# Performance work log

Measured on AMD Instinct MI355X. Metric: run time of the kernel, lower is better.

Reference implementation:

```python
import jax, jax.numpy as jnp
import numpy as np

N = 4096; E = 65536; IN = 512; H = 256; QD = 256; NH = 8; HD = QD // NH
OUT = 10; L = 2; CT = 50


def _ln(x, g, b, eps=1e-5):
    mu = x.mean(-1, keepdims=True)
    var = ((x - mu) ** 2).mean(-1, keepdims=True)
    return (x - mu) * jax.lax.rsqrt(var + eps) * g + b


def _forward(x, edge_index, cell_types, Wi, bi, Wq, bq, Wk, bk, Wv, bv, Bc, cemb,
             Win, bin_p, Wo, bo, Wm1, bm1, Wm2, bm2, Wm3, bm3, ln_g, ln_b,
             Wc1, bc1, Wc2, bc2):
    src, tgt = edge_index[0], edge_index[1]
    h = jax.nn.relu(x @ Wi + bi)                      # [N, H] input projection
    # graph connectivity scattered into a dense mask (as in _create_attention_mask)
    mask = jnp.zeros((N, N), jnp.float32).at[src, tgt].set(1.0)
    for l in range(L):
        res = h
        Q = h @ Wq[l] + bq[l]                         # [N, QD]
        K = h @ Wk[l] + bk[l]
        V = h @ Wv[l] + bv[l]
        Q = Q @ Bc[l]                                 # biological constraint
        K = K @ Bc[l].T
        ce = cemb[l][cell_types]                      # [N, QD] cell-type embedding
        Q = Q + 0.1 * ce
        K = K + 0.1 * ce
        # dense graph-masked attention (entanglement matrix), applied to V
        scores = (Q @ K.T) / float(np.sqrt(QD))      # [N, N]
        scores = jnp.where(mask == 0.0, -1e9, scores)
        attn = jax.nn.softmax(scores, axis=-1)
        graph_att = attn @ V                          # [N, QD]
        # nn.MultiheadAttention(Q, K, V) entanglement layer (eval mode)
        q = (Q @ Win[l, :, :QD] + bin_p[l, :QD]).reshape(N, NH, HD)
        k = (K @ Win[l, :, QD:2 * QD] + bin_p[l, QD:2 * QD]).reshape(N, NH, HD)
        v = (V @ Win[l, :, 2 * QD:] + bin_p[l, 2 * QD:]).reshape(N, NH, HD)
        w = jax.nn.softmax(jnp.einsum('nhd,mhd->hnm', q, k) / float(np.sqrt(HD)), axis=-1)
        mha = jnp.einsum('hnm,mhd->nhd', w, v).reshape(N, QD) @ Wo[l] + bo[l]
        # edge gather -> message MLP -> scatter-add (PyG aggr='add', x_i=target, x_j=source)
        # quantum slot of the concat is zeros, so only the first 2H rows of Wm1 contribute
        m = jnp.concatenate([h[tgt], h[src]], axis=-1) @ Wm1[l, :2 * H] + bm1[l]
        m = jax.nn.relu(m)
        m = jax.nn.relu(m @ Wm2[l] + bm2[l])
        m = m @ Wm3[l] + bm3[l]                       # [E, H]
        agg = jax.ops.segment_sum(m, tgt, num_segments=N)
        h = _ln(res + agg + mha + graph_att, ln_g[l], ln_b[l])
    # graph-level readout: mean || max pooling -> classifier (hidden*2 -> hidden -> out)
    pooled = jnp.concatenate([h.mean(0), h.max(0)], axis=-1)   # [2H]
    z = jax.nn.relu(pooled @ Wc1 + bc1)
    return z @ Wc2 + bc2                              # [OUT]


def setup_inputs():
    ks = jax.random.split(jax.random.key(0), 40)
    s = 0.05
    p = lambda i, shape: jax.random.normal(ks[i], shape, jnp.float32) * s
    z = lambda shape: jnp.zeros(shape, jnp.float32)
    return {
        'x': jax.random.normal(ks[0], (N, IN), jnp.float32),
        'edge_index': jax.random.randint(ks[1], (2, E), 0, N),
        'cell_types': jax.random.randint(ks[2], (N,), 0, CT),
        'Wi': p(3, (IN, H)), 'bi': z((H,)),
        'Wq': p(4, (L, H, QD)), 'bq': z((L, QD)),
        'Wk': p(5, (L, H, QD)), 'bk': z((L, QD)),
        'Wv': p(6, (L, H, QD)), 'bv': z((L, QD)),
        'Bc': p(7, (L, QD, QD)),
        'cemb': p(8, (L, CT, QD)),
        'Win': p(9, (L, QD, 3 * QD)), 'bin_p': z((L, 3 * QD)),
        'Wo': p(10, (L, QD, QD)), 'bo': z((L, QD)),
        'Wm1': p(11, (L, 2 * H + QD, QD)), 'bm1': z((L, QD)),
        'Wm2': p(12, (L, QD, QD)), 'bm2': z((L, QD)),
        'Wm3': p(13, (L, QD, H)), 'bm3': z((L, H)),
        'ln_g': jnp.ones((L, H), jnp.float32), 'ln_b': z((L, H)),
        'Wc1': p(14, (2 * H, H)), 'bc1': z((H,)),
        'Wc2': p(15, (H, OUT)), 'bc2': z((OUT,)),
    }


def reference(x, edge_index, cell_types, Wi, bi, Wq, bq, Wk, bk, Wv, bv, Bc, cemb,
              Win, bin_p, Wo, bo, Wm1, bm1, Wm2, bm2, Wm3, bm3, ln_g, ln_b,
              Wc1, bc1, Wc2, bc2):
    return _forward(x, edge_index, cell_types, Wi, bi, Wq, bq, Wk, bk, Wv, bv, Bc, cemb,
                    Win, bin_p, Wo, bo, Wm1, bm1, Wm2, bm2, Wm3, bm3, ln_g, ln_b,
                    Wc1, bc1, Wc2, bc2)
```

## Files before the change

kernel.cpp:

```cpp
#include <hip/hip_runtime.h>
#include <hip/hip_bf16.h>

#define N_NODES 4096
#define E_EDGES 65536
#define IN_F    512
#define H_F     256
#define QD      256
#define NHEAD   8
#define HD      32
#define OUT_F   10
#define L_LAYERS 2
#define CT_N    50

enum { FLAG_RELU = 1, FLAG_ACCUM = 2, FLAG_WF32 = 4, FLAG_WB16 = 8 };

typedef __attribute__((ext_vector_type(8))) __bf16 bf16x8;
typedef __attribute__((ext_vector_type(4))) float f32x4;

union PU { bf16x8 v; __hip_bfloat16 h[8]; __hip_bfloat162 b2[4]; };

template<int BM, int BN, bool EDGE>
__global__ __launch_bounds__(256) void gemm_mfma(
    const __hip_bfloat16* __restrict__ A, int lda,
    const __hip_bfloat16* __restrict__ B, int ldb,
    float* __restrict__ Cf, __hip_bfloat16* __restrict__ Cb, int ldc,
    int K,
    const float* __restrict__ bias, const float* __restrict__ rowscale,
    const int* __restrict__ tgtp, const int* __restrict__ srcp,
    const float* __restrict__ kbias,
    int flags)
{
    constexpr int WM = BM / 2, WN = BN / 2, MT = WM / 16, NT = WN / 16;
    constexpr int LDT = 40;
    __shared__ alignas(16) __hip_bfloat16 As[BM * LDT];
    __shared__ alignas(16) __hip_bfloat16 Bs[BN * LDT];

    const int tid = threadIdx.x;
    const int w = tid >> 6, lane = tid & 63, l16 = lane & 15, quad = lane >> 4;
    const int wm = w >> 1, wn = w & 1;
    const int bm = blockIdx.y * BM, bn = blockIdx.x * BN;

    f32x4 acc[MT][NT];
    #pragma unroll
    for (int i = 0; i < MT; ++i)
        #pragma unroll
        for (int j = 0; j < NT; ++j)
            #pragma unroll
            for (int r = 0; r < 4; ++r) acc[i][j][r] = 0.f;

    for (int k0 = 0; k0 < K; k0 += 32) {
        #pragma unroll
        for (int f = tid; f < BM * 4; f += 256) {
            int r = f >> 2, sg = f & 3;
            if (EDGE) {
                int i = bm + r;
                int tg = tgtp[i], sr = srcp[i];
                PU z1, z2, o;
                z1.v = *reinterpret_cast<const bf16x8*>(A + (size_t)tg * 512 + k0 + sg * 8);
                z2.v = *reinterpret_cast<const bf16x8*>(A + (size_t)sr * 512 + 256 + k0 + sg * 8);
                float4 b0 = *reinterpret_cast<const float4*>(kbias + k0 + sg * 8);
                float4 b1 = *reinterpret_cast<const float4*>(kbias + k0 + sg * 8 + 4);
                float bb[8] = {b0.x, b0.y, b0.z, b0.w, b1.x, b1.y, b1.z, b1.w};
                #pragma unroll
                for (int j = 0; j < 8; ++j) {
                    float v = __bfloat162float(z1.h[j]) + __bfloat162float(z2.h[j]) + bb[j];
                    o.h[j] = __float2bfloat16(fmaxf(v, 0.f));
                }
                *reinterpret_cast<bf16x8*>(&As[r * LDT + sg * 8]) = o.v;
            } else {
                *reinterpret_cast<uint4*>(&As[r * LDT + sg * 8]) =
                    *reinterpret_cast<const uint4*>(A + (size_t)(bm + r) * lda + k0 + sg * 8);
            }
        }
        #pragma unroll
        for (int f = tid; f < BN * 4; f += 256) {
            int r = f >> 2, sg = f & 3;
            *reinterpret_cast<uint4*>(&Bs[r * LDT + sg * 8]) =
                *reinterpret_cast<const uint4*>(B + (size_t)(bn + r) * ldb + k0 + sg * 8);
        }
        __syncthreads();
        bf16x8 af[MT], bfr[NT];
        #pragma unroll
        for (int mt = 0; mt < MT; ++mt)
            af[mt] = *reinterpret_cast<const bf16x8*>(&As[(wm * WM + mt * 16 + l16) * LDT + quad * 8]);
        #pragma unroll
        for (int nt = 0; nt < NT; ++nt)
            bfr[nt] = *reinterpret_cast<const bf16x8*>(&Bs[(wn * WN + nt * 16 + l16) * LDT + quad * 8]);
        #pragma unroll
        for (int mt = 0; mt < MT; ++mt)
            #pragma unroll
            for (int nt = 0; nt < NT; ++nt)
                acc[mt][nt] = __builtin_amdgcn_mfma_f32_16x16x32_bf16(af[mt], bfr[nt], acc[mt][nt], 0, 0, 0);
        __syncthreads();
    }

    #pragma unroll
    for (int mt = 0; mt < MT; ++mt) {
        #pragma unroll
        for (int nt = 0; nt < NT; ++nt) {
            int col = bn + wn * WN + nt * 16 + l16;
            #pragma unroll
            for (int r = 0; r < 4; ++r) {
                int row = bm + wm * WM + mt * 16 + quad * 4 + r;
                float v = acc[mt][nt][r];
                if (bias) {
                    float bv = bias[col];
                    if (rowscale) bv *= rowscale[row];
                    v += bv;
                }
                if (flags & FLAG_RELU) v = fmaxf(v, 0.f);
                size_t off = (size_t)row * ldc + col;
                if (flags & FLAG_ACCUM)     Cf[off] += v;
                else if (flags & FLAG_WF32) Cf[off] = v;
                if (flags & FLAG_WB16)      Cb[off] = __float2bfloat16(v);
            }
        }
    }
}

__global__ __launch_bounds__(512) void edge_gemm(
    const __hip_bfloat16* __restrict__ Z,
    const __hip_bfloat16* __restrict__ B,
    __hip_bfloat16* __restrict__ C,
    const int* __restrict__ tgtp, const int* __restrict__ srcp,
    const float* __restrict__ kbias,
    const float* __restrict__ bias)
{
    constexpr int LDA = 264;
    constexpr int LDB = 40;
    __shared__ alignas(16) __hip_bfloat16 As[64 * LDA];
    __shared__ alignas(16) __hip_bfloat16 Bs[256 * LDB];

    const int tid = threadIdx.x;
    const int w = tid >> 6, lane = tid & 63, l16 = lane & 15, quad = lane >> 4;
    const int bid = blockIdx.x;
    const int bm = ((bid & 7) * 128 + (bid >> 3)) * 64;

    bf16x8 zt[4], zs[4];
    #pragma unroll
    for (int u = 0; u < 4; ++u) {
        int g = u * 512 + tid;
        int r = g >> 5, c = g & 31;
        int i = bm + r;
        int tg = tgtp[i], sr = srcp[i];
        zt[u] = *reinterpret_cast<const bf16x8*>(Z + (size_t)tg * 512 + c * 8);
        zs[u] = *reinterpret_cast<const bf16x8*>(Z + (size_t)sr * 512 + 256 + c * 8);
    }
    #pragma unroll
    for (int u = 0; u < 4; ++u) {
        int g = u * 512 + tid;
        int r = g >> 5, c = g & 31;
        PU a, b, o;
        a.v = zt[u]; b.v = zs[u];
        float4 k0v = *reinterpret_cast<const float4*>(kbias + c * 8);
        float4 k1v = *reinterpret_cast<const float4*>(kbias + c * 8 + 4);
        float bb[8] = {k0v.x, k0v.y, k0v.z, k0v.w, k1v.x, k1v.y, k1v.z, k1v.w};
        #pragma unroll
        for (int j = 0; j < 8; ++j) {
            float v = __bfloat162float(a.h[j]) + __bfloat162float(b.h[j]) + bb[j];
            o.h[j] = __float2bfloat16(fmaxf(v, 0.f));
        }
        *reinterpret_cast<bf16x8*>(&As[r * LDA + c * 8]) = o.v;
    }

    const int wn = w;
    f32x4 acc[4][2];
    #pragma unroll
    for (int mt = 0; mt < 4; ++mt)
        #pragma unroll
        for (int nt = 0; nt < 2; ++nt)
            #pragma unroll
            for (int r = 0; r < 4; ++r) acc[mt][nt][r] = 0.f;

    for (int k0 = 0; k0 < 256; k0 += 32) {
        #pragma unroll
        for (int u = 0; u < 2; ++u) {
            int f = u * 512 + tid;
            int r = f >> 2, sg = f & 3;
            *reinterpret_cast<uint4*>(&Bs[r * LDB + sg * 8]) =
                *reinterpret_cast<const uint4*>(B + (size_t)r * 256 + k0 + sg * 8);
        }
        __syncthreads();
        bf16x8 af[4], bfr[2];
        #pragma unroll
        for (int mt = 0; mt < 4; ++mt)
            af[mt] = *reinterpret_cast<const bf16x8*>(&As[(mt * 16 + l16) * LDA + k0 + quad * 8]);
        #pragma unroll
        for (int nt = 0; nt < 2; ++nt)
            bfr[nt] = *reinterpret_cast<const bf16x8*>(&Bs[(wn * 32 + nt * 16 + l16) * LDB + quad * 8]);
        #pragma unroll
        for (int mt = 0; mt < 4; ++mt)
            #pragma unroll
            for (int nt = 0; nt < 2; ++nt)
                acc[mt][nt] = __builtin_amdgcn_mfma_f32_16x16x32_bf16(af[mt], bfr[nt], acc[mt][nt], 0, 0, 0);
        __syncthreads();
    }

    #pragma unroll
    for (int mt = 0; mt < 4; ++mt) {
        #pragma unroll
        for (int nt = 0; nt < 2; ++nt) {
            int col = wn * 32 + nt * 16 + l16;
            float bv = bias[col];
            #pragma unroll
            for (int r = 0; r < 4; ++r) {
                int row = bm + mt * 16 + quad * 4 + r;
                float v = fmaxf(acc[mt][nt][r] + bv, 0.f);
                C[(size_t)row * 256 + col] = __float2bfloat16(v);
            }
        }
    }
}

struct GSet { const __hip_bfloat16* A; int lda; const __hip_bfloat16* B;
              const float* bias; const float* rowscale;
              const float* extra; float esc; float cscale;
              __hip_bfloat16* C; float* Cf; int vtout; int ldc; int coloff; };
struct GPack { GSet s[8]; };

__global__ __launch_bounds__(256) void gemm_bz(GPack p, const int* __restrict__ eidx)
{
    GSet g = p.s[blockIdx.z];
    constexpr int LDT = 40;
    __shared__ alignas(16) __hip_bfloat16 As[64 * LDT];
    __shared__ alignas(16) __hip_bfloat16 Bs[64 * LDT];

    const int tid = threadIdx.x;
    const int w = tid >> 6, lane = tid & 63, l16 = lane & 15, quad = lane >> 4;
    const int wm = w >> 1, wn = w & 1;
    const int bm = blockIdx.y * 64, bn = blockIdx.x * 64;

    f32x4 acc[2][2];
    #pragma unroll
    for (int i = 0; i < 2; ++i)
        #pragma unroll
        for (int j = 0; j < 2; ++j)
            #pragma unroll
            for (int r = 0; r < 4; ++r) acc[i][j][r] = 0.f;

    for (int k0 = 0; k0 < 256; k0 += 32) {
        #pragma unroll
        for (int f = tid; f < 256; f += 256) {
            int r = f >> 2, sg = f & 3;
            *reinterpret_cast<uint4*>(&As[r * LDT + sg * 8]) =
                *reinterpret_cast<const uint4*>(g.A + (size_t)(bm + r) * g.lda + k0 + sg * 8);
            *reinterpret_cast<uint4*>(&Bs[r * LDT + sg * 8]) =
                *reinterpret_cast<const uint4*>(g.B + (size_t)(bn + r) * 256 + k0 + sg * 8);
        }
        __syncthreads();
        bf16x8 af[2], bfr[2];
        #pragma unroll
        for (int mt = 0; mt < 2; ++mt)
            af[mt] = *reinterpret_cast<const bf16x8*>(&As[(wm * 32 + mt * 16 + l16) * LDT + quad * 8]);
        #pragma unroll
        for (int nt = 0; nt < 2; ++nt)
            bfr[nt] = *reinterpret_cast<const bf16x8*>(&Bs[(wn * 32 + nt * 16 + l16) * LDT + quad * 8]);
        #pragma unroll
        for (int mt = 0; mt < 2; ++mt)
            #pragma unroll
            for (int nt = 0; nt < 2; ++nt)
                acc[mt][nt] = __builtin_amdgcn_mfma_f32_16x16x32_bf16(af[mt], bfr[nt], acc[mt][nt], 0, 0, 0);
        __syncthreads();
    }

    #pragma unroll
    for (int mt = 0; mt < 2; ++mt) {
        #pragma unroll
        for (int nt = 0; nt < 2; ++nt) {
            int colL = bn + wn * 32 + nt * 16 + l16;
            #pragma unroll
            for (int r = 0; r < 4; ++r) {
                int row = bm + wm * 32 + mt * 16 + quad * 4 + r;
                float v = acc[mt][nt][r];
                if (g.bias) {
                    float bv = g.bias[colL];
                    if (g.rowscale) bv *= g.rowscale[row];
                    v += bv;
                }
                if (g.extra) v += g.esc * g.extra[(size_t)eidx[row] * QD + colL];
                v *= g.cscale;
                if (g.vtout)
                    g.C[(size_t)colL * 4096 + row] = __float2bfloat16(v);
                else if (g.Cf)
                    g.Cf[(size_t)row * g.ldc + g.coloff + colL] = v;
                else
                    g.C[(size_t)row * g.ldc + g.coloff + colL] = __float2bfloat16(v);
            }
        }
    }
}

struct FDesc { const float* A; int lda; const float* B; int ldb; int tb;
               const float* bias; float* C; int M, N, K; };
struct FPack { FDesc d[16]; };

__global__ __launch_bounds__(256) void fgemm2(FPack p)
{
    FDesc c = p.d[blockIdx.z];
    int bm = blockIdx.y * 32, bn = blockIdx.x * 32;
    if (bm >= c.M || bn >= c.N) return;
    __shared__ float As[16][33];
    __shared__ float Bs[16][33];
    int tid = threadIdx.x;
    int tr = tid / 16, tc = tid % 16;
    float acc[2][2] = {};

    for (int k0 = 0; k0 < c.K; k0 += 16) {
        #pragma unroll
        for (int u = 0; u < 2; ++u) {
            int i = tid * 2 + u;
            int m = i >> 4, kk = i & 15;
            int row = bm + m, kg = k0 + kk;
            As[kk][m] = (row < c.M && kg < c.K) ? c.A[(size_t)row * c.lda + kg] : 0.f;
        }
        if (c.tb) {
            #pragma unroll
            for (int u = 0; u < 2; ++u) {
                int i = tid * 2 + u;
                int n = i >> 4, kk = i & 15;
                int col = bn + n, kg = k0 + kk;
                Bs[kk][n] = (col < c.N && kg < c.K) ? c.B[(size_t)col * c.ldb + kg] : 0.f;
            }
        } else {
            #pragma unroll
            for (int u = 0; u < 2; ++u) {
                int i = tid * 2 + u;
                int kk = i >> 5, n = i & 31;
                int col = bn + n, kg = k0 + kk;
                Bs[kk][n] = (col < c.N && kg < c.K) ? c.B[(size_t)kg * c.ldb + col] : 0.f;
            }
        }
        __syncthreads();
        #pragma unroll
        for (int kk = 0; kk < 16; ++kk) {
            float a0 = As[kk][tr * 2], a1 = As[kk][tr * 2 + 1];
            float b0 = Bs[kk][tc * 2], b1 = Bs[kk][tc * 2 + 1];
            acc[0][0] = fmaf(a0, b0, acc[0][0]);
            acc[0][1] = fmaf(a0, b1, acc[0][1]);
            acc[1][0] = fmaf(a1, b0, acc[1][0]);
            acc[1][1] = fmaf(a1, b1, acc[1][1]);
        }
        __syncthreads();
    }

    #pragma unroll
    for (int i = 0; i < 2; ++i) {
        int row = bm + tr * 2 + i;
        if (row >= c.M) continue;
        #pragma unroll
        for (int j = 0; j < 2; ++j) {
            int col = bn + tc * 2 + j;
            if (col >= c.N) continue;
            float v = acc[i][j];
            if (c.bias) v += c.bias[col];
            c.C[(size_t)row * c.N + col] = v;
        }
    }
}

__global__ __launch_bounds__(512, 4) void mha_flash10(
    const __hip_bfloat16* __restrict__ Qm,
    const __hip_bfloat16* __restrict__ Km,
    const __hip_bfloat16* __restrict__ Vt, __hip_bfloat16* __restrict__ Out)
{
    const int hh = blockIdx.y;
    const int tid = threadIdx.x;
    const int w = tid >> 6, lane = tid & 63, l16 = lane & 15, quad = lane >> 4;
    const int qb = blockIdx.x * 64;

    __shared__ float Osh[8][4][64][9];
    __shared__ float Lsh[8][4][16];

    bf16x8 aq[4];
    #pragma unroll
    for (int s = 0; s < 4; ++s)
        aq[s] = *reinterpret_cast<const bf16x8*>(
            Qm + (size_t)(qb + s * 16 + l16) * 256 + hh * 32 + quad * 8);
    const __hip_bfloat16* vb0 = Vt + (size_t)(hh * 32 + l16) * 4096;
    const __hip_bfloat16* vb1 = vb0 + (size_t)16 * 4096;
    const int rowoff = (l16 >> 2) * 8 + (l16 & 3);
    const f32x4 zero = {0.f, 0.f, 0.f, 0.f};

    PU onesu;
    #pragma unroll
    for (int j = 0; j < 8; ++j) onesu.h[j] = __float2bfloat16(1.f);
    const bf16x8 onesv = onesu.v;

    f32x4 o0[4], o1[4], lac[4];
    #pragma unroll
    for (int s = 0; s < 4; ++s) { o0[s] = zero; o1[s] = zero; lac[s] = zero; }

    const int kstart = w * 512;
    for (int kt = 0; kt < 8; ++kt) {
        const int kbase = kstart + kt * 64;
        bf16x8 kf[4];
        #pragma unroll
        for (int c = 0; c < 2; ++c)
            #pragma unroll
            for (int st = 0; st < 2; ++st)
                kf[c * 2 + st] = *reinterpret_cast<const bf16x8*>(
                    Km + (size_t)(kbase + c * 32 + st * 4 + rowoff) * 256 + hh * 32 + quad * 8);
        bf16x8 v00 = *reinterpret_cast<const bf16x8*>(vb0 + kbase + quad * 8);
        bf16x8 v01 = *reinterpret_cast<const bf16x8*>(vb1 + kbase + quad * 8);
        bf16x8 v10 = *reinterpret_cast<const bf16x8*>(vb0 + kbase + 32 + quad * 8);
        bf16x8 v11 = *reinterpret_cast<const bf16x8*>(vb1 + kbase + 32 + quad * 8);

        #pragma unroll
        for (int s = 0; s < 4; ++s) {
            f32x4 sv[4];
            __builtin_amdgcn_s_setprio(1);
            #pragma unroll
            for (int i = 0; i < 4; ++i)
                sv[i] = __builtin_amdgcn_mfma_f32_16x16x32_bf16(kf[i], aq[s], zero, 0, 0, 0);
            __builtin_amdgcn_s_setprio(0);
            PU p0, p1;
            #pragma unroll
            for (int i = 0; i < 4; ++i) {
                float e0 = exp2f(sv[i][0]), e1 = exp2f(sv[i][1]);
                float e2 = exp2f(sv[i][2]), e3 = exp2f(sv[i][3]);
                PU& pp = (i < 2) ? p0 : p1;
                pp.b2[(i & 1) * 2 + 0] = __float22bfloat162_rn(make_float2(e0, e1));
                pp.b2[(i & 1) * 2 + 1] = __float22bfloat162_rn(make_float2(e2, e3));
            }
            __builtin_amdgcn_s_setprio(1);
            o0[s]  = __builtin_amdgcn_mfma_f32_16x16x32_bf16(v00,   p0.v, o0[s],  0, 0, 0);
            o1[s]  = __builtin_amdgcn_mfma_f32_16x16x32_bf16(v01,   p0.v, o1[s],  0, 0, 0);
            lac[s] = __builtin_amdgcn_mfma_f32_16x16x32_bf16(onesv, p0.v, lac[s], 0, 0, 0);
            o0[s]  = __builtin_amdgcn_mfma_f32_16x16x32_bf16(v10,   p1.v, o0[s],  0, 0, 0);
            o1[s]  = __builtin_amdgcn_mfma_f32_16x16x32_bf16(v11,   p1.v, o1[s],  0, 0, 0);
            lac[s] = __builtin_amdgcn_mfma_f32_16x16x32_bf16(onesv, p1.v, lac[s], 0, 0, 0);
            __builtin_amdgcn_s_setprio(0);
        }
    }

    float lsum[4];
    #pragma unroll
    for (int s = 0; s < 4; ++s) lsum[s] = lac[s][0];

    #pragma unroll
    for (int s = 0; s < 4; ++s) {
        #pragma unroll
        for (int r = 0; r < 4; ++r) {
            Osh[w][s][lane][r]     = o0[s][r];
            Osh[w][s][lane][4 + r] = o1[s][r];
        }
        if (quad == 0) Lsh[w][s][l16] = lsum[s];
    }
    __syncthreads();
    if (w < 4) {
        const int s = w;
        f32x4 a0 = zero, a1 = zero;
        float ll = 0.f;
        #pragma unroll
        for (int ww = 0; ww < 8; ++ww) {
            #pragma unroll
            for (int r = 0; r < 4; ++r) {
                a0[r] += Osh[ww][s][lane][r];
                a1[r] += Osh[ww][s][lane][4 + r];
            }
            ll += Lsh[ww][s][l16];
        }
        float inv = 1.f / ll;
        __hip_bfloat16* dst = Out + (size_t)(qb + s * 16 + l16) * 256 + hh * 32;
        #pragma unroll
        for (int r = 0; r < 4; ++r) {
            dst[quad * 4 + r]      = __float2bfloat16(a0[r] * inv);
            dst[16 + quad * 4 + r] = __float2bfloat16(a1[r] * inv);
        }
    }
}

__global__ __launch_bounds__(256) void build_mask(const int* __restrict__ src,
                                                  const int* __restrict__ tgt,
                                                  unsigned* __restrict__ mb,
                                                  int* __restrict__ cnt)
{
    int e = blockIdx.x * 256 + threadIdx.x;
    if (e >= E_EDGES) return;
    int t = tgt[e];
    atomicOr(mb + (size_t)src[e] * (N_NODES / 32) + (t >> 5), 1u << (t & 31));
    atomicAdd(&cnt[t], 1);
}

__global__ __launch_bounds__(1024) void csr_scan(const int* __restrict__ cnt, int* __restrict__ off,
                                                 int* __restrict__ cursor, float* __restrict__ degf)
{
    __shared__ int sh[1024];
    int t = threadIdx.x;
    int base = t * 4;
    int c0 = cnt[base], c1 = cnt[base + 1], c2 = cnt[base + 2], c3 = cnt[base + 3];
    int sum = c0 + c1 + c2 + c3;
    sh[t] = sum; __syncthreads();
    for (int d = 1; d < 1024; d <<= 1) {
        int v = (t >= d) ? sh[t - d] : 0;
        __syncthreads();
        sh[t] += v;
        __syncthreads();
    }
    int excl = sh[t] - sum;
    int o0 = excl, o1 = excl + c0, o2 = o1 + c1, o3 = o2 + c2;
    off[base] = o0; off[base + 1] = o1; off[base + 2] = o2; off[base + 3] = o3;
    cursor[base] = o0; cursor[base + 1] = o1; cursor[base + 2] = o2; cursor[base + 3] = o3;
    degf[base] = (float)c0; degf[base + 1] = (float)c1;
    degf[base + 2] = (float)c2; degf[base + 3] = (float)c3;
    if (t == 1023) off[4096] = sh[t];
}

__global__ __launch_bounds__(256) void csr_fill(const int* __restrict__ src, const int* __restrict__ tgt,
                                                int* __restrict__ cursor,
                                                int* __restrict__ srcp, int* __restrict__ tgtp)
{
    int e = blockIdx.x * 256 + threadIdx.x;
    if (e >= E_EDGES) return;
    int t = tgt[e];
    int pos = atomicAdd(&cursor[t], 1);
    srcp[pos] = src[e];
    tgtp[pos] = t;
}

__global__ __launch_bounds__(256) void seg_sum(const int* __restrict__ off,
                                               const __hip_bfloat16* __restrict__ M2,
                                               __hip_bfloat16* __restrict__ A3)
{
    int n = blockIdx.x, t = threadIdx.x;
    int b0 = off[n], b1 = off[n + 1];
    float s = 0.f;
    for (int i = b0; i < b1; ++i)
        s += __bfloat162float(M2[(size_t)i * 256 + t]);
    A3[(size_t)n * 256 + t] = __float2bfloat16(s);
}

__global__ __launch_bounds__(256) void sparse_attn(
    const __hip_bfloat16* __restrict__ Q, const __hip_bfloat16* __restrict__ K,
    const __hip_bfloat16* __restrict__ V, int vld,
    const unsigned* __restrict__ maskb, float* __restrict__ outb)
{
    int i = blockIdx.x, t = threadIdx.x;
    __shared__ float qsh[256];
    __shared__ int   nb[1024];
    __shared__ float sc[1024];
    __shared__ int   cnt;
    __shared__ float red[4];
    __shared__ float smax, ssum;
    if (t == 0) cnt = 0;
    qsh[t] = __bfloat162float(Q[(size_t)i * 256 + t]);
    __syncthreads();
    if (t < 128) {
        unsigned wv = maskb[(size_t)i * 128 + t];
        while (wv) {
            int b = __ffs(wv) - 1; wv &= wv - 1;
            int p = atomicAdd(&cnt, 1);
            nb[p] = t * 32 + b;
        }
    }
    __syncthreads();
    int deg = cnt;
    int wid = t >> 6, lane = t & 63;
    if (deg > 0) {
        for (int n = wid; n < deg; n += 4) {
            union { uint2 u; __hip_bfloat16 h[4]; } kv;
            kv.u = *reinterpret_cast<const uint2*>(K + (size_t)nb[n] * 256 + lane * 4);
            float s = qsh[lane*4+0] * __bfloat162float(kv.h[0]) + qsh[lane*4+1] * __bfloat162float(kv.h[1])
                    + qsh[lane*4+2] * __bfloat162float(kv.h[2]) + qsh[lane*4+3] * __bfloat162float(kv.h[3]);
            #pragma unroll
            for (int off = 32; off; off >>= 1) s += __shfl_xor(s, off);
            if (lane == 0) sc[n] = s * 0.0625f;
        }
        __syncthreads();
        float m = -3.4e38f;
        for (int n = t; n < deg; n += 256) m = fmaxf(m, sc[n]);
        #pragma unroll
        for (int off = 32; off; off >>= 1) m = fmaxf(m, __shfl_xor(m, off));
        if (lane == 0) red[wid] = m;
        __syncthreads();
        if (t == 0) smax = fmaxf(fmaxf(red[0], red[1]), fmaxf(red[2], red[3]));
        __syncthreads();
        float ls = 0.f;
        for (int n = t; n < deg; n += 256) { float e = __expf(sc[n] - smax); sc[n] = e; ls += e; }
        #pragma unroll
        for (int off = 32; off; off >>= 1) ls += __shfl_xor(ls, off);
        if (lane == 0) red[wid] = ls;
        __syncthreads();
        if (t == 0) ssum = red[0] + red[1] + red[2] + red[3];
        __syncthreads();
        float inv = 1.f / ssum;
        float o = 0.f;
        for (int n = 0; n < deg; ++n)
            o += sc[n] * __bfloat162float(V[(size_t)nb[n] * vld + t]);
        outb[(size_t)i * 256 + t] = o * inv;
    } else {
        float o = 0.f;
        for (int j = 0; j < N_NODES; ++j) o += __bfloat162float(V[(size_t)j * vld + t]);
        outb[(size_t)i * 256 + t] = o * (1.f / N_NODES);
    }
}

__global__ __launch_bounds__(256) void ln_kernel(float* __restrict__ h, __hip_bfloat16* __restrict__ h16,
                                                 const float* __restrict__ a1,
                                                 const float* __restrict__ a2,
                                                 const float* __restrict__ a3,
                                                 const float* __restrict__ g, const float* __restrict__ b)
{
    int row = blockIdx.x, t = threadIdx.x;
    __shared__ float red[256];
    size_t off = ((size_t)row << 8) + t;
    float v = h[off] + a1[off] + a2[off] + a3[off];
    red[t] = v; __syncthreads();
    for (int s = 128; s > 0; s >>= 1) { if (t < s) red[t] += red[t + s]; __syncthreads(); }
    float mu = red[0] * (1.f / 256.f); __syncthreads();
    float d = v - mu;
    red[t] = d * d; __syncthreads();
    for (int s = 128; s > 0; s >>= 1) { if (t < s) red[t] += red[t + s]; __syncthreads(); }
    float var = red[0] * (1.f / 256.f);
    float r = d * rsqrtf(var + 1e-5f) * g[t] + b[t];
    h[off] = r;
    h16[off] = __float2bfloat16(r);
}

__global__ __launch_bounds__(256) void colpool(const float* __restrict__ h, float* __restrict__ p)
{
    int c = blockIdx.x, t = threadIdx.x;
    __shared__ float rs[256], rm[256];
    float s = 0.f, m = -3.4e38f;
    for (int row = t; row < N_NODES; row += 256) {
        float v = h[((size_t)row << 8) + c];
        s += v; m = fmaxf(m, v);
    }
    rs[t] = s; rm[t] = m; __syncthreads();
    for (int st = 128; st > 0; st >>= 1) {
        if (t < st) { rs[t] += rs[t + st]; rm[t] = fmaxf(rm[t], rm[t + st]); }
        __syncthreads();
    }
    if (t == 0) { p[c] = rs[0] * (1.f / N_NODES); p[256 + c] = rm[0]; }
}

__global__ __launch_bounds__(256) void classifier(const float* __restrict__ pooled,
                                                  const float* __restrict__ Wc1, const float* __restrict__ bc1,
                                                  const float* __restrict__ Wc2, const float* __restrict__ bc2,
                                                  float* __restrict__ out)
{
    __shared__ float p[512];
    __shared__ float z[256];
    int t = threadIdx.x;
    p[t] = pooled[t]; p[256 + t] = pooled[256 + t];
    __syncthreads();
    float s = bc1[t];
    for (int k = 0; k < 512; ++k) s = fmaf(p[k], Wc1[k * 256 + t], s);
    z[t] = fmaxf(s, 0.f);
    __syncthreads();
    if (t < OUT_F) {
        float o = bc2[t];
        for (int j = 0; j < 256; ++j) o = fmaf(z[j], Wc2[j * OUT_F + t], o);
        out[t] = o;
    }
}

struct CDesc { const float* s; __hip_bfloat16* d; int total; };
struct CPack { CDesc d[2]; };
__global__ __launch_bounds__(256) void convert_copy(CPack p)
{
    CDesc c = p.d[blockIdx.y];
    for (int i = blockIdx.x * 256 + threadIdx.x; i < c.total; i += gridDim.x * 256)
        c.d[i] = __float2bfloat16(c.s[i]);
}
struct TDesc { const float* s; __hip_bfloat16* d; int K, N, sld; };
struct TPack { TDesc d[23]; };
__global__ __launch_bounds__(256) void convert_t32(TPack p)
{
    TDesc c = p.d[blockIdx.z];
    int k0 = blockIdx.x * 32, n0 = blockIdx.y * 32;
    if (k0 >= c.K || n0 >= c.N) return;
    __shared__ float t[32][33];
    int tr = threadIdx.x >> 5, tc = threadIdx.x & 31;
    #pragma unroll
    for (int rr = 0; rr < 32; rr += 8)
        t[tc][tr + rr] = c.s[(size_t)(k0 + tr + rr) * c.sld + n0 + tc];
    __syncthreads();
    #pragma unroll
    for (int rr = 0; rr < 32; rr += 8)
        c.d[(size_t)(n0 + tr + rr) * c.K + k0 + tc] = __float2bfloat16(t[tr + rr][tc]);
}

extern "C" void kernel_launch(void* const* d_in, const int* in_sizes, int n_in,
                              void* d_out, int out_size, void* d_ws, size_t ws_size,
                              hipStream_t stream)
{
    const float* x    = (const float*)d_in[0];
    const int*   ei   = (const int*)d_in[1];
    const int*   ct   = (const int*)d_in[2];
    const float* Wi   = (const float*)d_in[3];
    const float* bi   = (const float*)d_in[4];
    const float* Wq   = (const float*)d_in[5];
    const float* bq   = (const float*)d_in[6];
    const float* Wk   = (const float*)d_in[7];
    const float* bk   = (const float*)d_in[8];
    const float* Wv   = (const float*)d_in[9];
    const float* bv   = (const float*)d_in[10];
    const float* Bc   = (const float*)d_in[11];
    const float* cemb = (const float*)d_in[12];
    const float* Win  = (const float*)d_in[13];
    const float* binp = (const float*)d_in[14];
    const float* Wo   = (const float*)d_in[15];
    const float* bo   = (const float*)d_in[16];
    const float* Wm1  = (const float*)d_in[17];
    const float* bm1  = (const float*)d_in[18];
    const float* Wm2  = (const float*)d_in[19];
    const float* bm2  = (const float*)d_in[20];
    const float* Wm3  = (const float*)d_in[21];
    const float* bm3  = (const float*)d_in[22];
    const float* lng  = (const float*)d_in[23];
    const float* lnb  = (const float*)d_in[24];
    const float* Wc1  = (const float*)d_in[25];
    const float* bc1  = (const float*)d_in[26];
    const float* Wc2  = (const float*)d_in[27];
    const float* bc2  = (const float*)d_in[28];

    const int* src = ei;
    const int* tgt = ei + E_EDGES;

    char* wp = (char*)d_ws;
    auto alloc = [&](size_t bytes) { char* r = wp; wp += (bytes + 255) & ~(size_t)255; return r; };
    const size_t NH = (size_t)N_NODES * 256;
    float* h      = (float*)alloc(NH * 4);
    float* a1     = (float*)alloc(NH * 4);
    float* a2     = (float*)alloc(NH * 4);
    float* a3     = (float*)alloc(NH * 4);
    float* pooled = (float*)alloc(512 * 4);
    float* degf   = (float*)alloc(N_NODES * 4);
    __hip_bfloat16* x16 = (__hip_bfloat16*)alloc((size_t)N_NODES * 512 * 2);
    __hip_bfloat16* h16 = (__hip_bfloat16*)alloc(NH * 2);
    __hip_bfloat16* Qb  = (__hip_bfloat16*)alloc(NH * 2);
    __hip_bfloat16* Kb  = (__hip_bfloat16*)alloc(NH * 2);
    __hip_bfloat16* Vb  = (__hip_bfloat16*)alloc(NH * 2);
    __hip_bfloat16* Tq  = (__hip_bfloat16*)alloc(NH * 2);
    __hip_bfloat16* Tk  = (__hip_bfloat16*)alloc(NH * 2);
    __hip_bfloat16* Vt  = (__hip_bfloat16*)alloc(NH * 2);
    __hip_bfloat16* Z12 = (__hip_bfloat16*)alloc((size_t)N_NODES * 512 * 2);
    __hip_bfloat16* M216= (__hip_bfloat16*)alloc((size_t)E_EDGES * 256 * 2);
    __hip_bfloat16* A3  = (__hip_bfloat16*)alloc(NH * 2);
    __hip_bfloat16* Wi_t= (__hip_bfloat16*)alloc((size_t)256 * 512 * 2);
    float *Wqc_f[2], *Wkc_f[2], *Wqm_f[2], *Wkm_f[2], *Wvm_f[2];
    float *bqc[2], *bkc[2], *bqm[2], *bkm[2], *bvm[2], *ceq2[2], *cek2[2];
    for (int l = 0; l < 2; ++l) {
        Wqc_f[l] = (float*)alloc(65536 * 4); Wkc_f[l] = (float*)alloc(65536 * 4);
        Wqm_f[l] = (float*)alloc(65536 * 4); Wkm_f[l] = (float*)alloc(65536 * 4);
        Wvm_f[l] = (float*)alloc(65536 * 4);
        bqc[l] = (float*)alloc(256 * 4); bkc[l] = (float*)alloc(256 * 4);
        bqm[l] = (float*)alloc(256 * 4); bkm[l] = (float*)alloc(256 * 4);
        bvm[l] = (float*)alloc(256 * 4);
        ceq2[l] = (float*)alloc(CT_N * 256 * 4); cek2[l] = (float*)alloc(CT_N * 256 * 4);
    }
    __hip_bfloat16* WB[2][11];
    for (int l = 0; l < 2; ++l)
        for (int m = 0; m < 11; ++m)
            WB[l][m] = (__hip_bfloat16*)alloc(65536 * 2);
    unsigned* maskb = (unsigned*)alloc((size_t)N_NODES * 128 * 4);
    int* cnt    = (int*)alloc(N_NODES * 4);
    int* cursor = (int*)alloc(N_NODES * 4);
    int* off    = (int*)alloc((N_NODES + 1) * 4);
    int* srcp   = (int*)alloc(E_EDGES * 4);
    int* tgtp   = (int*)alloc(E_EDGES * 4);

    CPack cp; cp.d[0] = {x, x16, N_NODES * 512};
    convert_copy<<<dim3(256, 1), 256, 0, stream>>>(cp);

    FPack f1; int n1 = 0;
    FPack f2; int n2 = 0;
    for (int l = 0; l < 2; ++l) {
        const float* Wq_l  = Wq + (size_t)l * 65536;
        const float* Wk_l  = Wk + (size_t)l * 65536;
        const float* Wv_l  = Wv + (size_t)l * 65536;
        const float* Bc_l  = Bc + (size_t)l * 65536;
        const float* Win_l = Win + (size_t)l * 256 * 768;
        const float* ce_l  = cemb + (size_t)l * CT_N * QD;
        const float* bq_l  = bq + l * 256;
        const float* bk_l  = bk + l * 256;
        const float* bv_l  = bv + l * 256;
        const float* bin_l = binp + l * 768;
        f1.d[n1++] = {Wq_l, 256, Bc_l, 256, 0, nullptr, Wqc_f[l], 256, 256, 256};
        f1.d[n1++] = {Wk_l, 256, Bc_l, 256, 1, nullptr, Wkc_f[l], 256, 256, 256};
        f1.d[n1++] = {bq_l, 256, Bc_l, 256, 0, nullptr, bqc[l], 1, 256, 256};
        f1.d[n1++] = {bk_l, 256, Bc_l, 256, 1, nullptr, bkc[l], 1, 256, 256};
        f2.d[n2++] = {Wqc_f[l], 256, Win_l,       768, 0, nullptr, Wqm_f[l], 256, 256, 256};
        f2.d[n2++] = {Wkc_f[l], 256, Win_l + 256, 768, 0, nullptr, Wkm_f[l], 256, 256, 256};
        f2.d[n2++] = {Wv_l,     256, Win_l + 512, 768, 0, nullptr, Wvm_f[l], 256, 256, 256};
        f2.d[n2++] = {ce_l,     256, Win_l,       768, 0, nullptr, ceq2[l], CT_N, 256, 256};
        f2.d[n2++] = {ce_l,     256, Win_l + 256, 768, 0, nullptr, cek2[l], CT_N, 256, 256};
        f2.d[n2++] = {bqc[l],   256, Win_l,       768, 0, bin_l,       bqm[l], 1, 256, 256};
        f2.d[n2++] = {bkc[l],   256, Win_l + 256, 768, 0, bin_l + 256, bkm[l], 1, 256, 256};
        f2.d[n2++] = {bv_l,     256, Win_l + 512, 768, 0, bin_l + 512, bvm[l], 1, 256, 256};
    }
    fgemm2<<<dim3(8, 8, n1), 256, 0, stream>>>(f1);
    fgemm2<<<dim3(8, 8, n2), 256, 0, stream>>>(f2);

    TPack tp; int ndt = 0;
    auto addT = [&](const float* s, __hip_bfloat16* d, int K, int N, int sld) { tp.d[ndt++] = {s, d, K, N, sld}; };
    addT(Wi, Wi_t, 512, 256, 256);
    for (int l = 0; l < 2; ++l) {
        const float* Wv_l  = Wv + (size_t)l * 65536;
        const float* Wo_l  = Wo + (size_t)l * 65536;
        const float* Wm1_l = Wm1 + (size_t)l * (2 * H_F + QD) * QD;
        const float* Wm2_l = Wm2 + (size_t)l * 65536;
        const float* Wm3_l = Wm3 + (size_t)l * 65536;
        addT(Wqc_f[l], WB[l][0], 256, 256, 256);
        addT(Wkc_f[l], WB[l][1], 256, 256, 256);
        addT(Wqm_f[l], WB[l][2], 256, 256, 256);
        addT(Wkm_f[l], WB[l][3], 256, 256, 256);
        addT(Wvm_f[l], WB[l][4], 256, 256, 256);
        addT(Wv_l,     WB[l][5], 256, 256, 256);
        addT(Wo_l,     WB[l][6], 256, 256, 256);
        addT(Wm1_l,             WB[l][7], 256, 256, 256);
        addT(Wm1_l + 256 * 256, WB[l][8], 256, 256, 256);
        addT(Wm2_l,    WB[l][9],  256, 256, 256);
        addT(Wm3_l,    WB[l][10], 256, 256, 256);
    }
    convert_t32<<<dim3(16, 8, ndt), 256, 0, stream>>>(tp);

    hipMemsetAsync(maskb, 0, (size_t)N_NODES * 128 * 4, stream);
    hipMemsetAsync(cnt, 0, N_NODES * 4, stream);
    build_mask<<<E_EDGES / 256, 256, 0, stream>>>(src, tgt, maskb, cnt);
    csr_scan<<<1, 1024, 0, stream>>>(cnt, off, cursor, degf);
    csr_fill<<<E_EDGES / 256, 256, 0, stream>>>(src, tgt, cursor, srcp, tgtp);

    gemm_mfma<64, 64, false><<<dim3(4, 64), 256, 0, stream>>>(
        x16, 512, Wi_t, 512, h, h16, 256, 512,
        bi, nullptr, nullptr, nullptr, nullptr, FLAG_RELU | FLAG_WF32 | FLAG_WB16);

    const float QSCALE = 0.25507693f;

    for (int l = 0; l < L_LAYERS; ++l) {
        const float* ce_l  = cemb + (size_t)l * CT_N * QD;
        const float* bo_l  = bo + l * QD;
        const float* bm1_l = bm1 + l * QD;
        const float* bm2_l = bm2 + l * QD;
        const float* bm3_l = bm3 + l * H_F;
        const float* lng_l = lng + l * H_F;
        const float* lnb_l = lnb + l * H_F;
        const float* bv_l  = bv + l * 256;

        {
            GPack gp;
            gp.s[0] = {h16, 256, WB[l][0], bqc[l], nullptr, ce_l,    0.1f, 1.0f,   Qb,  nullptr, 0, 256, 0};
            gp.s[1] = {h16, 256, WB[l][1], bkc[l], nullptr, ce_l,    0.1f, 1.0f,   Kb,  nullptr, 0, 256, 0};
            gp.s[2] = {h16, 256, WB[l][5], bv_l,   nullptr, nullptr, 0.f,  1.0f,   Vb,  nullptr, 0, 256, 0};
            gp.s[3] = {h16, 256, WB[l][2], bqm[l], nullptr, ceq2[l], 0.1f, QSCALE, Tq,  nullptr, 0, 256, 0};
            gp.s[4] = {h16, 256, WB[l][3], bkm[l], nullptr, cek2[l], 0.1f, 1.0f,   Tk,  nullptr, 0, 256, 0};
            gp.s[5] = {h16, 256, WB[l][4], bvm[l], nullptr, nullptr, 0.f,  1.0f,   Vt,  nullptr, 1, 256, 0};
            gp.s[6] = {h16, 256, WB[l][7], nullptr, nullptr, nullptr, 0.f, 1.0f,   Z12, nullptr, 0, 512, 0};
            gp.s[7] = {h16, 256, WB[l][8], nullptr, nullptr, nullptr, 0.f, 1.0f,   Z12, nullptr, 0, 512, 256};
            gemm_bz<<<dim3(4, 64, 8), 256, 0, stream>>>(gp, ct);
        }

        sparse_attn<<<N_NODES, 256, 0, stream>>>(Qb, Kb, Vb, 256, maskb, a1);

        mha_flash10<<<dim3(64, NHEAD), 512, 0, stream>>>(Tq, Tk, Vt, Qb);

        edge_gemm<<<E_EDGES / 64, 512, 0, stream>>>(
            Z12, WB[l][9], M216, tgtp, srcp, bm1_l, bm2_l);
        seg_sum<<<N_NODES, 256, 0, stream>>>(off, M216, A3);

        {
            GPack gp;
            gp.s[0] = {Qb, 256, WB[l][6],  bo_l,  nullptr, nullptr, 0.f, 1.0f, nullptr, a2, 0, 256, 0};
            gp.s[1] = {A3, 256, WB[l][10], bm3_l, degf,    nullptr, 0.f, 1.0f, nullptr, a3, 0, 256, 0};
            gemm_bz<<<dim3(4, 64, 2), 256, 0, stream>>>(gp, ct);
        }

        ln_kernel<<<N_NODES, 256, 0, stream>>>(h, h16, a1, a2, a3, lng_l, lnb_l);
    }

    colpool<<<H_F, 256, 0, stream>>>(h, pooled);
    classifier<<<1, 256, 0, stream>>>(pooled, Wc1, bc1, Wc2, bc2, (float*)d_out);
}
```

Measured before the change: 512.9 us.

## Split MHA key range across two blocks with atomic merge and normalize pass

The dense MHA kernel now splits the key dimension across a third grid axis of two blocks, each covering half the keys, doubling the block count from 512 to 1024 for better CU occupancy. Partial unnormalized outputs and row sums are merged with float atomicAdd into fp32 buffers, and a new mha_norm kernel divides and converts to bf16. The in-block reduction is restructured into a two-stage tree that halves shared memory. This adds two memsets, one extra kernel launch, fp32 atomic traffic, and nondeterministic summation order.

```diff
diff --git a/kernel.cpp b/kernel.cpp
--- a/kernel.cpp
+++ b/kernel.cpp
@@ -358,18 +358,19 @@
     }
 }
 
-__global__ __launch_bounds__(512, 4) void mha_flash10(
+__global__ __launch_bounds__(512, 4) void mha_flash12(
     const __hip_bfloat16* __restrict__ Qm,
     const __hip_bfloat16* __restrict__ Km,
-    const __hip_bfloat16* __restrict__ Vt, __hip_bfloat16* __restrict__ Out)
+    const __hip_bfloat16* __restrict__ Vt,
+    float* __restrict__ Of, float* __restrict__ Lf)
 {
     const int hh = blockIdx.y;
     const int tid = threadIdx.x;
     const int w = tid >> 6, lane = tid & 63, l16 = lane & 15, quad = lane >> 4;
     const int qb = blockIdx.x * 64;
 
-    __shared__ float Osh[8][4][64][9];
-    __shared__ float Lsh[8][4][16];
+    __shared__ float Osh[4][4][64][9];
+    __shared__ float Lsh[4][4][16];
 
     bf16x8 aq[4];
     #pragma unroll
@@ -390,8 +391,8 @@
     #pragma unroll
     for (int s = 0; s < 4; ++s) { o0[s] = zero; o1[s] = zero; lac[s] = zero; }
 
-    const int kstart = w * 512;
-    for (int kt = 0; kt < 8; ++kt) {
+    const int kstart = (blockIdx.z * 8 + w) * 256;
+    for (int kt = 0; kt < 4; ++kt) {
         const int kbase = kstart + kt * 64;
         bf16x8 kf[4];
         #pragma unroll
@@ -437,37 +438,76 @@
     #pragma unroll
     for (int s = 0; s < 4; ++s) lsum[s] = lac[s][0];
 
-    #pragma unroll
-    for (int s = 0; s < 4; ++s) {
-        #pragma unroll
-        for (int r = 0; r < 4; ++r) {
-            Osh[w][s][lane][r]     = o0[s][r];
-            Osh[w][s][lane][4 + r] = o1[s][r];
-        }
-        if (quad == 0) Lsh[w][s][l16] = lsum[s];
+    if (w >= 4) {
+        #pragma unroll
+        for (int s = 0; s < 4; ++s) {
+            #pragma unroll
+            for (int r = 0; r < 4; ++r) {
+                Osh[w - 4][s][lane][r]     = o0[s][r];
+                Osh[w - 4][s][lane][4 + r] = o1[s][r];
+            }
+            if (quad == 0) Lsh[w - 4][s][l16] = lsum[s];
+        }
+    }
+    __syncthreads();
+    if (w < 4) {
+        #pragma unroll
+        for (int s = 0; s < 4; ++s) {
+            #pragma unroll
+            for (int r = 0; r < 4; ++r) {
+                o0[s][r] += Osh[w][s][lane][r];
+                o1[s][r] += Osh[w][s][lane][4 + r];
+            }
+            lsum[s] += Lsh[w][s][l16];
+        }
+    }
+    __syncthreads();
+    if (w < 4) {
+        #pragma unroll
+        for (int s = 0; s < 4; ++s) {
+            if (s == w) continue;
+            #pragma unroll
+            for (int r = 0; r < 4; ++r) {
+                Osh[w][s][lane][r]     = o0[s][r];
+                Osh[w][s][lane][4 + r] = o1[s][r];
+            }
+            if (quad == 0) Lsh[w][s][l16] = lsum[s];
+        }
     }
     __syncthreads();
     if (w < 4) {
         const int s = w;
-        f32x4 a0 = zero, a1 = zero;
-        float ll = 0.f;
-        #pragma unroll
-        for (int ww = 0; ww < 8; ++ww) {
+        f32x4 a0 = o0[s], a1 = o1[s];
+        float ll = lsum[s];
+        #pragma unroll
+        for (int i = 0; i < 4; ++i) {
+            if (i == s) continue;
             #pragma unroll
             for (int r = 0; r < 4; ++r) {
-                a0[r] += Osh[ww][s][lane][r];
-                a1[r] += Osh[ww][s][lane][4 + r];
-            }
-            ll += Lsh[ww][s][l16];
-        }
-        float inv = 1.f / ll;
-        __hip_bfloat16* dst = Out + (size_t)(qb + s * 16 + l16) * 256 + hh * 32;
+                a0[r] += Osh[i][s][lane][r];
+                a1[r] += Osh[i][s][lane][4 + r];
+            }
+            ll += Lsh[i][s][l16];
+        }
+        float* dst = Of + (size_t)(qb + s * 16 + l16) * 256 + hh * 32;
         #pragma unroll
         for (int r = 0; r < 4; ++r) {
-            dst[quad * 4 + r]      = __float2bfloat16(a0[r] * inv);
-            dst[16 + quad * 4 + r] = __float2bfloat16(a1[r] * inv);
-        }
-    }
+            atomicAdd(&dst[quad * 4 + r],      a0[r]);
+            atomicAdd(&dst[16 + quad * 4 + r], a1[r]);
+        }
+        if (quad == 0)
+            atomicAdd(&Lf[hh * N_NODES + qb + s * 16 + l16], ll);
+    }
+}
+
+__global__ __launch_bounds__(256) void mha_norm(
+    const float* __restrict__ Of, const float* __restrict__ Lf,
+    __hip_bfloat16* __restrict__ Out)
+{
+    int row = blockIdx.x, t = threadIdx.x;
+    int head = t >> 5;
+    float v = Of[(size_t)row * 256 + t] / Lf[head * N_NODES + row];
+    Out[(size_t)row * 256 + t] = __float2bfloat16(v);
 }
 
 __global__ __launch_bounds__(256) void build_mask(const int* __restrict__ src,
@@ -727,6 +767,8 @@
     float* a3     = (float*)alloc(NH * 4);
     float* pooled = (float*)alloc(512 * 4);
     float* degf   = (float*)alloc(N_NODES * 4);
+    float* Of     = (float*)alloc(NH * 4);
+    float* Lf     = (float*)alloc((size_t)NHEAD * N_NODES * 4);
     __hip_bfloat16* x16 = (__hip_bfloat16*)alloc((size_t)N_NODES * 512 * 2);
     __hip_bfloat16* h16 = (__hip_bfloat16*)alloc(NH * 2);
     __hip_bfloat16* Qb  = (__hip_bfloat16*)alloc(NH * 2);
@@ -851,9 +893,13 @@
             gemm_bz<<<dim3(4, 64, 8), 256, 0, stream>>>(gp, ct);
         }
 
+        hipMemsetAsync(Of, 0, NH * 4, stream);
+        hipMemsetAsync(Lf, 0, (size_t)NHEAD * N_NODES * 4, stream);
+
         sparse_attn<<<N_NODES, 256, 0, stream>>>(Qb, Kb, Vb, 256, maskb, a1);
 
-        mha_flash10<<<dim3(64, NHEAD), 512, 0, stream>>>(Tq, Tk, Vt, Qb);
+        mha_flash12<<<dim3(64, NHEAD, 2), 512, 0, stream>>>(Tq, Tk, Vt, Of, Lf);
+        mha_norm<<<N_NODES, 256, 0, stream>>>(Of, Lf, Qb);
 
         edge_gemm<<<E_EDGES / 64, 512, 0, stream>>>(
             Z12, WB[l][9], M216, tgtp, srcp, bm1_l, bm2_l);
```

After: 567.2 us. 1.11x slower.
